# Optimization experiments

Measured on AMD Instinct MI355X. Metric: run time of the kernel, lower is better.

Reference implementation:

```python
import jax, jax.numpy as jnp
import numpy as np

N_POINTS, N_GRIDS, K = 1024, 512, 7


def setup_inputs() -> dict:
    key = jax.random.key(0)
    k1, k2, k3, k4 = jax.random.split(key, 4)
    points = jax.random.uniform(k1, (N_POINTS, 3), dtype=jnp.float32) * 2.0 - 1.0
    volume_centers = jax.random.uniform(k2, (N_GRIDS, 3), dtype=jnp.float32) * 2.0 - 1.0
    min_s, max_s = 0.01, 1.0
    scales = jax.random.uniform(k3, (N_GRIDS,), dtype=jnp.float32) * (max_s - min_s) + min_s
    mosaic_sdf_values = jax.random.normal(k4, (N_GRIDS, K, K, K), dtype=jnp.float32)
    return {"points": points, "volume_centers": volume_centers,
            "scales": scales, "mosaic_sdf_values": mosaic_sdf_values}


def reference(points, volume_centers, scales, mosaic_sdf_values):
    G, k = mosaic_sdf_values.shape[0], mosaic_sdf_values.shape[1]
    # scaled relative positions: (N, G, 3)
    rel = (points[:, None, :] - volume_centers[None, :, :]) / scales[None, :, None]
    # grid node coordinates in [0,1]^3, flattened: (k^3, 3)
    lin = jnp.linspace(0.0, 1.0, k, dtype=points.dtype)
    gx, gy, gz = jnp.meshgrid(lin, lin, lin, indexing='ij')
    coords = jnp.stack([gx, gy, gz], axis=-1).reshape(-1, 3)
    # squared distance ||rel - coord||^2 expanded -> avoids (N,G,k^3,3) materialization
    d2 = (jnp.sum(rel * rel, axis=-1)[..., None]
          - 2.0 * jnp.einsum('ngd,cd->ngc', rel, coords)
          + jnp.sum(coords * coords, axis=-1)[None, None, :])  # (N, G, k^3)
    dist = jnp.sqrt(jnp.maximum(d2, 0.0))
    # original: weight = dist where dist <= 1 else 0, normalized over grid nodes
    w = jnp.where(dist <= 1.0, dist, 0.0)
    s = jnp.sum(w, axis=-1, keepdims=True)
    w = jnp.where(s > 0, w / jnp.where(s == 0, 1.0, s), 0.0)  # nan_to_num(0) equivalent
    vals = mosaic_sdf_values.reshape(G, -1)  # (G, k^3)
    interp = jnp.einsum('ngc,gc->ng', w, vals)  # (N, G)
    # per-grid blend weight: relu(1 - ||rel||), normalized over grids
    pdist = jnp.linalg.norm(rel, axis=-1)  # (N, G)
    gw = jax.nn.relu(1.0 - pdist)
    gs = jnp.sum(gw, axis=-1, keepdims=True)
    gw = jnp.where(gs > 0, gw / jnp.where(gs == 0, 1.0, gs), 0.0)
    return jnp.sum(interp * gw, axis=-1)  # (N,)
```

## Files before the change

kernel.cpp:

```cpp
#include <hip/hip_runtime.h>


#define NPTS   1024
#define NGRIDS 512
#define TPB    512
#define NBLK   512
#define ROWF   344
#define STEP   (1.0f / 6.0f)
#define FSQRT(x) __builtin_amdgcn_sqrtf(x)

__global__ __launch_bounds__(TPB) void msdf_fused(
    const float* __restrict__ points,
    const float* __restrict__ centers,
    const float* __restrict__ scales,
    const float* __restrict__ vals,
    float* __restrict__ out)
{
    __shared__ float  s_v[32][ROWF];
    __shared__ float4 s_pair[8][128];
    __shared__ unsigned short s_gid[8][128];
    __shared__ int   s_c[8];
    __shared__ float s_d[8];
    __shared__ float s_red[8][2];

    const int bid  = blockIdx.x;
    const int t    = threadIdx.x;
    const int w    = t >> 6;
    const int lane = t & 63;
    const int grp  = t >> 4;
    const int sub  = t & 15;

    float* s_cen = &s_v[0][0];
    float* s_scl = s_cen + 1536;
    {
        float4* dst = (float4*)s_cen;
        const float4* c4 = (const float4*)centers;
        const float4* s4 = (const float4*)scales;
        dst[t] = (t < 384) ? c4[t] : s4[t - 384];
    }

    const int   n  = (bid << 1) + (w >> 2);
    const float px = points[n * 3 + 0];
    const float py = points[n * 3 + 1];
    const float pz = points[n * 3 + 2];
    __syncthreads();

    float dsum  = 0.0f;
    int   cbase = 0;
    #pragma unroll
    for (int r = 0; r < 2; ++r) {
        const int g = ((w & 3) << 7) + (r << 6) + lane;
        const float invs = 1.0f / s_scl[g];
        const float rx = (px - s_cen[g * 3 + 0]) * invs;
        const float ry = (py - s_cen[g * 3 + 1]) * invs;
        const float rz = (pz - s_cen[g * 3 + 2]) * invs;
        const float gwr = 1.0f - FSQRT(rx * rx + ry * ry + rz * rz);
        const bool  act = (gwr > 0.0f);
        const unsigned long long m = __ballot(act);
        if (act) {
            const int pos = cbase + (int)__popcll(m & ((1ull << lane) - 1ull));
            s_pair[w][pos] = make_float4(rx, ry, rz, gwr);
            s_gid[w][pos]  = (unsigned short)g;
            dsum += gwr;
        }
        cbase += (int)__popcll(m);
    }
    #pragma unroll
    for (int o = 32; o >= 1; o >>= 1) dsum += __shfl_xor(dsum, o);
    if (lane == 0) { s_c[w] = cbase; s_d[w] = dsum; }
    __syncthreads();

    const int o1 = s_c[0];
    const int o2 = o1 + s_c[1];
    const int o3 = o2 + s_c[2];
    const int o4 = o3 + s_c[3];
    const int o5 = o4 + s_c[4];
    const int o6 = o5 + s_c[5];
    const int o7 = o6 + s_c[6];
    const int CT = o7 + s_c[7];
    const float den0 = s_d[0] + s_d[1] + s_d[2] + s_d[3];
    const float den1 = s_d[4] + s_d[5] + s_d[6] + s_d[7];

    float acc0 = 0.0f, acc1 = 0.0f;
    if (CT > 0) {
        const int nch = (CT + 31) >> 5;
        float  rbuf[22];
        float4 pr;
        int    gid, seg;

        #define FETCH(a_) {                                               \
            const int pc = ((a_) < CT) ? (a_) : (CT - 1);                 \
            seg = (pc >= o1) + (pc >= o2) + (pc >= o3) + (pc >= o4)       \
                + (pc >= o5) + (pc >= o6) + (pc >= o7);                   \
            const int b0 = (seg == 0) ? 0 : (seg == 1) ? o1               \
                         : (seg == 2) ? o2 : (seg == 3) ? o3              \
                         : (seg == 4) ? o4 : (seg == 5) ? o5              \
                         : (seg == 6) ? o6 : o7;                          \
            pr  = s_pair[seg][pc - b0];                                   \
            gid = (int)s_gid[seg][pc - b0]; }

        #define LOADROW() {                                               \
            const float* __restrict__ grow = vals + gid * 343;            \
            _Pragma("unroll")                                             \
            for (int k = 0; k < 21; ++k) rbuf[k] = grow[sub + 16 * k];    \
            rbuf[21] = (sub < 7) ? grow[336 + sub] : 0.0f; }

        FETCH(grp); LOADROW();
        float* __restrict__ myv = &s_v[grp][0];

        for (int c = 0; c < nch; ++c) {
            #pragma unroll
            for (int k = 0; k < 21; ++k) myv[sub + 16 * k] = rbuf[k];
            if (sub < 7) myv[336 + sub] = rbuf[21];

            const float4 prc  = pr;
            const int    segc = seg;
            const float  gw   = (32 * c + grp < CT) ? prc.w : 0.0f;

            if (c + 1 < nch) { FETCH(32 * (c + 1) + grp); LOADROW(); }

            float dz2[7];
            #pragma unroll
            for (int l = 0; l < 7; ++l) { const float d = prc.z - l * STEP; dz2[l] = d * d; }

            float ws = 0.0f, vs = 0.0f;
            #pragma unroll
            for (int rr = 0; rr < 3; ++rr) {
                const int rowid = sub + (rr << 4);
                const int i = (rowid * 9363) >> 16;
                const int j = rowid - i * 7;
                const float dxv = prc.x - (float)i * STEP;
                const float dyv = prc.y - (float)j * STEP;
                const float dxy = dxv * dxv + dyv * dyv;
                const float* __restrict__ vr = myv + rowid * 7;
                #pragma unroll
                for (int l = 0; l < 7; ++l) {
                    const float d2 = dxy + dz2[l];
                    const float wt = (d2 <= 1.0f) ? FSQRT(d2) : 0.0f;
                    ws += wt;
                    vs  = fmaf(wt, vr[l], vs);
                }
            }
            if (sub < 7) {
                const float dxv = prc.x - 1.0f;
                const float dyv = prc.y - 1.0f;
                const float dzv = prc.z - (float)sub * STEP;
                const float d2  = dxv * dxv + dyv * dyv + dzv * dzv;
                const float wt  = (d2 <= 1.0f) ? FSQRT(d2) : 0.0f;
                ws += wt;
                vs  = fmaf(wt, myv[336 + sub], vs);
            }
            #pragma unroll
            for (int o = 8; o >= 1; o >>= 1) {
                ws += __shfl_xor(ws, o);
                vs += __shfl_xor(vs, o);
            }
            const float interp = (ws > 0.0f) ? (vs / ws) : 0.0f;
            if (sub == 0) {
                const float contrib = interp * gw;
                if (segc < 4) acc0 += contrib;
                else          acc1 += contrib;
            }
        }
        #undef FETCH
        #undef LOADROW
    }

    #pragma unroll
    for (int o = 32; o >= 1; o >>= 1) {
        acc0 += __shfl_xor(acc0, o);
        acc1 += __shfl_xor(acc1, o);
    }
    if (lane == 0) { s_red[w][0] = acc0; s_red[w][1] = acc1; }
    __syncthreads();
    if (t < 2) {
        float nm = 0.0f;
        #pragma unroll
        for (int i = 0; i < 8; ++i) nm += s_red[i][t];
        const float dn = (t == 0) ? den0 : den1;
        out[(bid << 1) + t] = (dn > 0.0f) ? (nm / dn) : 0.0f;
    }
}

extern "C" void kernel_launch(void* const* d_in, const int* in_sizes, int n_in,
                              void* d_out, int out_size, void* d_ws, size_t ws_size,
                              hipStream_t stream) {
    const float* points  = (const float*)d_in[0];
    const float* centers = (const float*)d_in[1];
    const float* scales  = (const float*)d_in[2];
    const float* vals    = (const float*)d_in[3];
    float* out = (float*)d_out;

    msdf_fused<<<NBLK, TPB, 0, stream>>>(points, centers, scales, vals, out);
}
```

Before: 16.54 us.

## Read grid values directly from global memory and drop LDS staging

Removes the shared-memory staging of centers, scales and per-grid SDF rows. Centers and scales are now read straight from global memory, and the 343 values per grid are fetched directly inside the inner loop instead of being register-prefetched and copied to LDS. This frees about 44 KB of LDS per block and adds an occupancy hint to launch_bounds, so more blocks can be resident at once. In exchange it loses the explicit software prefetch, and the strided per-thread reads of 7 contiguous floats may coalesce poorly and leave load latency exposed.

```diff
diff --git a/kernel.cpp b/kernel.cpp
--- a/kernel.cpp
+++ b/kernel.cpp
@@ -5,18 +5,16 @@
 #define NGRIDS 512
 #define TPB    512
 #define NBLK   512
-#define ROWF   344
 #define STEP   (1.0f / 6.0f)
 #define FSQRT(x) __builtin_amdgcn_sqrtf(x)
 
-__global__ __launch_bounds__(TPB) void msdf_fused(
+__global__ __launch_bounds__(TPB, 4) void msdf_fused(
     const float* __restrict__ points,
     const float* __restrict__ centers,
     const float* __restrict__ scales,
     const float* __restrict__ vals,
     float* __restrict__ out)
 {
-    __shared__ float  s_v[32][ROWF];
     __shared__ float4 s_pair[8][128];
     __shared__ unsigned short s_gid[8][128];
     __shared__ int   s_c[8];
@@ -30,30 +28,20 @@
     const int grp  = t >> 4;
     const int sub  = t & 15;
 
-    float* s_cen = &s_v[0][0];
-    float* s_scl = s_cen + 1536;
-    {
-        float4* dst = (float4*)s_cen;
-        const float4* c4 = (const float4*)centers;
-        const float4* s4 = (const float4*)scales;
-        dst[t] = (t < 384) ? c4[t] : s4[t - 384];
-    }
-
     const int   n  = (bid << 1) + (w >> 2);
     const float px = points[n * 3 + 0];
     const float py = points[n * 3 + 1];
     const float pz = points[n * 3 + 2];
-    __syncthreads();
 
     float dsum  = 0.0f;
     int   cbase = 0;
     #pragma unroll
     for (int r = 0; r < 2; ++r) {
         const int g = ((w & 3) << 7) + (r << 6) + lane;
-        const float invs = 1.0f / s_scl[g];
-        const float rx = (px - s_cen[g * 3 + 0]) * invs;
-        const float ry = (py - s_cen[g * 3 + 1]) * invs;
-        const float rz = (pz - s_cen[g * 3 + 2]) * invs;
+        const float invs = 1.0f / scales[g];
+        const float rx = (px - centers[g * 3 + 0]) * invs;
+        const float ry = (py - centers[g * 3 + 1]) * invs;
+        const float rz = (pz - centers[g * 3 + 2]) * invs;
         const float gwr = 1.0f - FSQRT(rx * rx + ry * ry + rz * rz);
         const bool  act = (gwr > 0.0f);
         const unsigned long long m = __ballot(act);
@@ -82,88 +70,59 @@
     const float den1 = s_d[4] + s_d[5] + s_d[6] + s_d[7];
 
     float acc0 = 0.0f, acc1 = 0.0f;
-    if (CT > 0) {
-        const int nch = (CT + 31) >> 5;
-        float  rbuf[22];
-        float4 pr;
-        int    gid, seg;
+    for (int a = grp; a < CT; a += 32) {
+        const int seg = (a >= o1) + (a >= o2) + (a >= o3) + (a >= o4)
+                      + (a >= o5) + (a >= o6) + (a >= o7);
+        const int b0  = (seg == 0) ? 0 : (seg == 1) ? o1
+                      : (seg == 2) ? o2 : (seg == 3) ? o3
+                      : (seg == 4) ? o4 : (seg == 5) ? o5
+                      : (seg == 6) ? o6 : o7;
+        const float4 pr  = s_pair[seg][a - b0];
+        const int    gid = (int)s_gid[seg][a - b0];
+        const float* __restrict__ grow = vals + gid * 343;
 
-        #define FETCH(a_) {                                               \
-            const int pc = ((a_) < CT) ? (a_) : (CT - 1);                 \
-            seg = (pc >= o1) + (pc >= o2) + (pc >= o3) + (pc >= o4)       \
-                + (pc >= o5) + (pc >= o6) + (pc >= o7);                   \
-            const int b0 = (seg == 0) ? 0 : (seg == 1) ? o1               \
-                         : (seg == 2) ? o2 : (seg == 3) ? o3              \
-                         : (seg == 4) ? o4 : (seg == 5) ? o5              \
-                         : (seg == 6) ? o6 : o7;                          \
-            pr  = s_pair[seg][pc - b0];                                   \
-            gid = (int)s_gid[seg][pc - b0]; }
+        float dz2[7];
+        #pragma unroll
+        for (int l = 0; l < 7; ++l) { const float d = pr.z - l * STEP; dz2[l] = d * d; }
 
-        #define LOADROW() {                                               \
-            const float* __restrict__ grow = vals + gid * 343;            \
-            _Pragma("unroll")                                             \
-            for (int k = 0; k < 21; ++k) rbuf[k] = grow[sub + 16 * k];    \
-            rbuf[21] = (sub < 7) ? grow[336 + sub] : 0.0f; }
-
-        FETCH(grp); LOADROW();
-        float* __restrict__ myv = &s_v[grp][0];
-
-        for (int c = 0; c < nch; ++c) {
+        float ws = 0.0f, vs = 0.0f;
+        #pragma unroll
+        for (int rr = 0; rr < 3; ++rr) {
+            const int rowid = sub + (rr << 4);
+            const int i = (rowid * 9363) >> 16;
+            const int j = rowid - i * 7;
+            const float dxv = pr.x - (float)i * STEP;
+            const float dyv = pr.y - (float)j * STEP;
+            const float dxy = dxv * dxv + dyv * dyv;
+            const float* __restrict__ vr = grow + rowid * 7;
             #pragma unroll
-            for (int k = 0; k < 21; ++k) myv[sub + 16 * k] = rbuf[k];
-            if (sub < 7) myv[336 + sub] = rbuf[21];
-
-            const float4 prc  = pr;
-            const int    segc = seg;
-            const float  gw   = (32 * c + grp < CT) ? prc.w : 0.0f;
-
-            if (c + 1 < nch) { FETCH(32 * (c + 1) + grp); LOADROW(); }
-
-            float dz2[7];
-            #pragma unroll
-            for (int l = 0; l < 7; ++l) { const float d = prc.z - l * STEP; dz2[l] = d * d; }
-
-            float ws = 0.0f, vs = 0.0f;
-            #pragma unroll
-            for (int rr = 0; rr < 3; ++rr) {
-                const int rowid = sub + (rr << 4);
-                const int i = (rowid * 9363) >> 16;
-                const int j = rowid - i * 7;
-                const float dxv = prc.x - (float)i * STEP;
-                const float dyv = prc.y - (float)j * STEP;
-                const float dxy = dxv * dxv + dyv * dyv;
-                const float* __restrict__ vr = myv + rowid * 7;
-                #pragma unroll
-                for (int l = 0; l < 7; ++l) {
-                    const float d2 = dxy + dz2[l];
-                    const float wt = (d2 <= 1.0f) ? FSQRT(d2) : 0.0f;
-                    ws += wt;
-                    vs  = fmaf(wt, vr[l], vs);
-                }
-            }
-            if (sub < 7) {
-                const float dxv = prc.x - 1.0f;
-                const float dyv = prc.y - 1.0f;
-                const float dzv = prc.z - (float)sub * STEP;
-                const float d2  = dxv * dxv + dyv * dyv + dzv * dzv;
-                const float wt  = (d2 <= 1.0f) ? FSQRT(d2) : 0.0f;
+            for (int l = 0; l < 7; ++l) {
+                const float d2 = dxy + dz2[l];
+                const float wt = (d2 <= 1.0f) ? FSQRT(d2) : 0.0f;
                 ws += wt;
-                vs  = fmaf(wt, myv[336 + sub], vs);
-            }
-            #pragma unroll
-            for (int o = 8; o >= 1; o >>= 1) {
-                ws += __shfl_xor(ws, o);
-                vs += __shfl_xor(vs, o);
-            }
-            const float interp = (ws > 0.0f) ? (vs / ws) : 0.0f;
-            if (sub == 0) {
-                const float contrib = interp * gw;
-                if (segc < 4) acc0 += contrib;
-                else          acc1 += contrib;
+                vs  = fmaf(wt, vr[l], vs);
             }
         }
-        #undef FETCH
-        #undef LOADROW
+        if (sub < 7) {
+            const float dxv = pr.x - 1.0f;
+            const float dyv = pr.y - 1.0f;
+            const float dzv = pr.z - (float)sub * STEP;
+            const float d2  = dxv * dxv + dyv * dyv + dzv * dzv;
+            const float wt  = (d2 <= 1.0f) ? FSQRT(d2) : 0.0f;
+            ws += wt;
+            vs  = fmaf(wt, grow[336 + sub], vs);
+        }
+        #pragma unroll
+        for (int o = 8; o >= 1; o >>= 1) {
+            ws += __shfl_xor(ws, o);
+            vs += __shfl_xor(vs, o);
+        }
+        const float interp = (ws > 0.0f) ? (vs / ws) : 0.0f;
+        if (sub == 0) {
+            const float contrib = interp * pr.w;
+            if (seg < 4) acc0 += contrib;
+            else         acc1 += contrib;
+        }
     }
 
     #pragma unroll
```

New measurement: 14.19 us, median of 2. 1.17x faster.
